# Kernel optimization log

Hardware: AMD Instinct MI355X
Metric: run time of the kernel (lower is better)

## Reference

```python
import jax, jax.numpy as jnp
import numpy as np
from itertools import combinations

N_QUBITS = 8
N_TRASH = 2
N_LAYERS = 4
BATCH = 32768
DIM = 2 ** N_QUBITS  # 256


def _cz_pairs():
    # same CZ pattern as layer() in the torch module; all pairs are distinct,
    # and CZ gates are diagonal and commute, so they fuse into one sign mask.
    pairs = list(combinations(range(N_TRASH), 2))
    for idx in range(N_TRASH):
        for i in range(N_TRASH):
            for j in range(N_TRASH + i, N_QUBITS, N_TRASH):
                pairs.append(((idx + i) % N_TRASH, j))
    return pairs


def _cz_layer_sign():
    bits = np.indices((2,) * N_QUBITS)  # [n_qubits, 2,...,2]; wire 0 = MSB (PennyLane order)
    sign = np.ones((2,) * N_QUBITS, np.float32)
    for a, b in _cz_pairs():
        sign = sign * (1.0 - 2.0 * (bits[a] * bits[b]).astype(np.float32))
    return jnp.asarray(sign)[None]  # broadcast over batch

_CZ_SIGN = _cz_layer_sign()


def _ry(state, theta, w):
    # RY(theta) on wire w, batched over leading axis. state: [B,2,...,2] complex64
    c = jnp.cos(theta / 2).astype(jnp.complex64)
    s = jnp.sin(theta / 2).astype(jnp.complex64)
    g = jnp.stack([jnp.stack([c, -s]), jnp.stack([s, c])])  # [2,2]
    out = jnp.tensordot(g, state, axes=((1,), (1 + w,)))
    return jnp.moveaxis(out, 0, 1 + w)


def _axis_vec(vals, w):
    shape = [1] * (N_QUBITS + 1)
    shape[1 + w] = 2
    return jnp.asarray(vals, dtype=jnp.complex64).reshape(shape)


def _apply_pauli(state, w, p):
    if p == 'X':
        return jnp.flip(state, axis=1 + w)
    if p == 'Y':
        return jnp.flip(state, axis=1 + w) * _axis_vec([-1j, 1j], w)
    return state * _axis_vec([1.0 + 0j, -1.0 + 0j], w)  # Z


def _forward(x, weights):
    # AmplitudeEmbedding(normalize=True)
    norm = jnp.sqrt(jnp.sum(x * x, axis=-1, keepdims=True))
    psi = (x / norm).astype(jnp.complex64).reshape((-1,) + (2,) * N_QUBITS)
    for l in range(N_LAYERS - 1):
        for q in range(N_QUBITS):
            psi = _ry(psi, weights[l * N_QUBITS + q], q)
        psi = psi * _CZ_SIGN  # all CZs of the layer fused into one diagonal
    base = (N_LAYERS - 1) * N_QUBITS
    for q in range(N_TRASH):  # last_layer: RY on trash qubits only
        psi = _ry(psi, weights[base + q], q)

    axes = tuple(range(1, N_QUBITS + 1))
    conj_psi = jnp.conj(psi)

    def ev(op_state):
        return jnp.sum(conj_psi * op_state, axis=axes).real.astype(jnp.float32)

    w0, w1 = 6, 7
    terms = [
        ev(_apply_pauli(psi, w0, 'X')),
        ev(_apply_pauli(psi, w0, 'Y')),
        ev(_apply_pauli(psi, w0, 'Z')),
        ev(_apply_pauli(psi, w1, 'X')),
        ev(_apply_pauli(psi, w1, 'Y')),
        ev(_apply_pauli(psi, w1, 'Z')),
        ev(_apply_pauli(_apply_pauli(psi, w0, 'X'), w1, 'X')),
        ev(_apply_pauli(_apply_pauli(psi, w0, 'Y'), w1, 'Y')),
        ev(_apply_pauli(_apply_pauli(psi, w0, 'Z'), w1, 'Z')),
    ]
    return jnp.stack(terms, axis=1)  # [B, 9]


def setup_inputs() -> dict:
    key = jax.random.key(0)
    kx, kw = jax.random.split(key)
    x = jax.random.normal(kx, (BATCH, DIM), dtype=jnp.float32)
    n_w = N_LAYERS * N_QUBITS - (N_QUBITS - N_TRASH)  # 26
    weights = jax.random.normal(kw, (n_w,), dtype=jnp.float32)
    return {'x': x, 'weights': weights}


def reference(x, weights):
    return _forward(x, weights)
```

## Files before the change

kernel.cpp:

```cpp
#include <hip/hip_runtime.h>
#include <math.h>

#define DIM 256
typedef float v2f  __attribute__((ext_vector_type(2)));
typedef _Float16 f16x8 __attribute__((ext_vector_type(8)));
typedef float f32x4 __attribute__((ext_vector_type(4)));

__device__ __forceinline__ v2f mk2(float a, float b) { v2f r; r.x = a; r.y = b; return r; }
__device__ __forceinline__ float rl(float v, int l) {
    return __uint_as_float(__builtin_amdgcn_readlane(__float_as_uint(v), l));
}

template<int B2>
__device__ __forceinline__ void ry_pk(v2f* v, float c, float s) {
#pragma unroll
    for (int p = 0; p < 16; ++p)
        if (!(p & (1 << B2))) {
            const int q = p | (1 << B2);
            v2f lo = v[p], hi = v[q];
            v[p] = c * lo - s * hi;
            v[q] = s * lo + c * hi;
        }
}
__device__ __forceinline__ void ry_intra(v2f* v, float c, float s) {
#pragma unroll
    for (int p = 0; p < 16; ++p) {
        float lo = v[p].x, hi = v[p].y;
        v[p].x = fmaf(-s, hi, c * lo);
        v[p].y = fmaf(s, lo, c * hi);
    }
}

__global__ __launch_bounds__(256) void qae_buildU(const float* __restrict__ w,
                                                  _Float16* __restrict__ uf) {
    __shared__ float4 lds4[2048];
    const int lane = threadIdx.x & 63;
    const int wid  = threadIdx.x >> 6;
    const int wave = blockIdx.x * 4 + wid;
    const int l3   = lane & 7;
    const int e    = lane >> 3;
    const int col  = wave * 8 + e;
    float4* W = lds4 + wid * 512 + e * 64;

    float h = 0.f;
    if (lane < 20) h = 0.5f * w[lane < 18 ? lane : lane + 4];
    const float cv = __cosf(h), sv = __sinf(h);
#define RYP(B2, slot) ry_pk<B2>(v, rl(cv, slot), rl(sv, slot))
#define RYI(slot)     ry_intra(v, rl(cv, slot), rl(sv, slot))

    const int a0 = (l3 >> 2) & 1, a1 = (l3 >> 1) & 1, a2 = l3 & 1;
    const int aa = a0 & a1, dd = a0 ^ a1;
    const float fE = (aa ^ (dd & a2)) ? -1.f : 1.f;
    const float fO = ((aa ^ (dd & a2)) ^ dd) ? -1.f : 1.f;
    const float pB = (__popc(l3) & 1) ? -1.f : 1.f;
    const v2f mA0 = mk2(fE, fO), mA1 = mk2(fO, fE);
    const v2f mBp = mk2(pB, -pB);

    v2f v[16];
#pragma unroll
    for (int p = 0; p < 16; ++p) v[p] = mk2(0.f, 0.f);
    if (((col >> 2) & 7) == l3) {
        const int p = 2 * (col >> 5) + ((col >> 1) & 1);
        if (col & 1) v[p].y = 1.f; else v[p].x = 1.f;
    }

    RYP(3, 0); RYP(2, 1); RYP(1, 2);
#pragma unroll
    for (int g = 0; g < 8; ++g)
        W[g * 8 + (l3 ^ g)] = make_float4(v[2*g].x, v[2*g].y, v[2*g+1].x, v[2*g+1].y);
#pragma unroll
    for (int k = 0; k < 8; ++k) {
        float4 f = W[l3 * 8 + (k ^ l3)];
        v[2*k] = mk2(f.x, f.y); v[2*k+1] = mk2(f.z, f.w);
    }
    RYP(3, 3); RYP(2, 4); RYP(1, 5); RYP(0, 6); RYI(7);
#pragma unroll
    for (int p = 0; p < 16; ++p) v[p] *= (__popc(p) & 1) ? mA1 : mA0;
    RYP(3, 11); RYP(2, 12); RYP(1, 13); RYP(0, 14); RYI(15);
#pragma unroll
    for (int k = 0; k < 8; ++k)
        W[l3 * 8 + (k ^ l3)] = make_float4(v[2*k].x, v[2*k].y, v[2*k+1].x, v[2*k+1].y);
#pragma unroll
    for (int g = 0; g < 8; ++g) {
        float4 f = W[g * 8 + (l3 ^ g)];
        v[2*g] = mk2(f.x, f.y); v[2*g+1] = mk2(f.z, f.w);
    }
    RYP(3, 8); RYP(2, 9); RYP(1, 10);
#pragma unroll
    for (int p = 0; p < 16; ++p) {
        const int b0 = (p >> 3) & 1, b1 = (p >> 2) & 1;
        if (b0 & b1)      v[p] = -v[p];
        else if (b0 ^ b1) v[p] *= (__popc(p & 3) & 1) ? -mBp : mBp;
    }
    RYP(3, 16); RYP(2, 17); RYP(0, 18); RYI(19);
#pragma unroll
    for (int p = 0; p < 16; ++p) {
        const int b0 = (p >> 3) & 1, b1 = (p >> 2) & 1;
        if (b0 & b1)      v[p] = -v[p];
        else if (b0 ^ b1) v[p] *= (__popc(p & 3) & 1) ? -mBp : mBp;
    }
#undef RYP
#undef RYI

    const int ks = col >> 5, j = col & 7, lfhi = ((col >> 3) & 3) << 4;
#pragma unroll
    for (int p = 0; p < 16; ++p) {
        const int mbase = ((p >> 1) << 5) | (l3 << 2) | ((p & 1) << 1);
        {   const int m = mbase, mt = m >> 4, lf = (m & 15) | lfhi;
            uf[(size_t)(((mt * 8 + ks) * 64 + lf) * 8 + j)] = (_Float16)v[p].x; }
        {   const int m = mbase | 1, mt = m >> 4, lf = (m & 15) | lfhi;
            uf[(size_t)(((mt * 8 + ks) * 64 + lf) * 8 + j)] = (_Float16)v[p].y; }
    }
}

__global__ __launch_bounds__(256) void qae_gemm(const float* __restrict__ x,
                                                const _Float16* __restrict__ uf,
                                                float* __restrict__ out, int batch) {
    __shared__ __align__(16) _Float16 Ut[16384];
    const int lane  = threadIdx.x & 63;
    const int wid   = threadIdx.x >> 6;
    const int strip = blockIdx.x * 4 + wid;
    const int bl = lane & 15, bq = lane >> 4;
    const int b  = strip * 16 + bl;
    const bool act = (b < batch);

    const float* xp = x + (size_t)b * DIM + bq * 8;
    f16x8 bf[8];
    float nrm = 0.f;
#pragma unroll
    for (int ks = 0; ks < 8; ++ks) {
        float4 f0 = make_float4(0.f, 0.f, 0.f, 0.f), f1 = f0;
        if (act) { f0 = *(const float4*)(xp + 32 * ks);
                   f1 = *(const float4*)(xp + 32 * ks + 4); }
        nrm += f0.x*f0.x + f0.y*f0.y + f0.z*f0.z + f0.w*f0.w
             + f1.x*f1.x + f1.y*f1.y + f1.z*f1.z + f1.w*f1.w;
        bf[ks][0] = (_Float16)f0.x; bf[ks][1] = (_Float16)f0.y;
        bf[ks][2] = (_Float16)f0.z; bf[ks][3] = (_Float16)f0.w;
        bf[ks][4] = (_Float16)f1.x; bf[ks][5] = (_Float16)f1.y;
        bf[ks][6] = (_Float16)f1.z; bf[ks][7] = (_Float16)f1.w;
    }

    float pX6 = 0, pX7 = 0, pXX = 0, pYY = 0, pZ6 = 0, pZ7 = 0, pZZ = 0;

#pragma unroll
    for (int ph = 0; ph < 4; ++ph) {
        __syncthreads();
        const float4* src = (const float4*)uf + (size_t)ph * 2048 + threadIdx.x;
        float4* dst = (float4*)Ut;
#pragma unroll
        for (int i = 0; i < 8; ++i)
            dst[i * 256 + threadIdx.x] = src[i * 256];
        __syncthreads();
#pragma unroll
        for (int mtl = 0; mtl < 4; ++mtl) {
            f32x4 acc = {0.f, 0.f, 0.f, 0.f};
#pragma unroll
            for (int ks = 0; ks < 8; ++ks) {
                f16x8 af = *(const f16x8*)(Ut + ((mtl * 8 + ks) * 64 + lane) * 8);
                acc = __builtin_amdgcn_mfma_f32_16x16x32_f16(af, bf[ks], acc, 0, 0, 0);
            }
            const float q0 = acc[0], q1 = acc[1], q2 = acc[2], q3 = acc[3];
            pX6 += q0 * q2 + q1 * q3;
            pX7 += q0 * q1 + q2 * q3;
            pXX += q0 * q3 + q1 * q2;
            pYY += q1 * q2 - q0 * q3;
            const float s0 = q0*q0, s1 = q1*q1, s2 = q2*q2, s3 = q3*q3;
            pZ6 += (s0 + s1) - (s2 + s3);
            pZ7 += (s0 - s1) + (s2 - s3);
            pZZ += (s0 - s1) - (s2 - s3);
        }
    }

#pragma unroll
    for (int m = 16; m <= 32; m <<= 1) {
        nrm += __shfl_xor(nrm, m);
        pX6 += __shfl_xor(pX6, m); pX7 += __shfl_xor(pX7, m);
        pXX += __shfl_xor(pXX, m); pYY += __shfl_xor(pYY, m);
        pZ6 += __shfl_xor(pZ6, m); pZ7 += __shfl_xor(pZ7, m);
        pZZ += __shfl_xor(pZZ, m);
    }

    if (act && bq == 0) {
        const float inv = 1.f / nrm;
        float* o = out + (size_t)b * 9;
        o[0] = 2.f * pX6 * inv;  o[1] = 0.f;  o[2] = pZ6 * inv;
        o[3] = 2.f * pX7 * inv;  o[4] = 0.f;  o[5] = pZ7 * inv;
        o[6] = 2.f * pXX * inv;  o[7] = 2.f * pYY * inv;  o[8] = pZZ * inv;
    }
}

extern "C" void kernel_launch(void* const* d_in, const int* in_sizes, int n_in,
                              void* d_out, int out_size, void* d_ws, size_t ws_size,
                              hipStream_t stream) {
    const float* x = (const float*)d_in[0];
    const float* w = (const float*)d_in[1];
    float* out = (float*)d_out;
    _Float16* uf = (_Float16*)d_ws;
    const int batch = in_sizes[0] / DIM;

    qae_buildU<<<8, 256, 0, stream>>>(w, uf);

    const int strips = (batch + 15) / 16;
    qae_gemm<<<(strips + 3) / 4, 256, 0, stream>>>(x, uf, out, batch);
}
```

Before: 92.63 us.

## Coalesce x loads through LDS staging and vectorize U-matrix fragment stores

The GEMM kernel now loads each 16-row strip of x with fully coalesced row-wise float4 reads, converts to fp16 into a per-wave LDS buffer, then reads the MFMA B fragments from LDS. Before, each lane read strided 32-byte pieces. The norm is now computed from the fp16-rounded values, a small accuracy change. buildU transposes its results through LDS so it can write 16-byte vector stores instead of scattered 2-byte stores. The change also sets launch_bounds occupancy to 2 and adds 32KB of LDS per block, which may limit occupancy.

```diff
diff --git a/kernel.cpp b/kernel.cpp
--- a/kernel.cpp
+++ b/kernel.cpp
@@ -4,6 +4,7 @@
 #define DIM 256
 typedef float v2f  __attribute__((ext_vector_type(2)));
 typedef _Float16 f16x8 __attribute__((ext_vector_type(8)));
+typedef _Float16 f16x4 __attribute__((ext_vector_type(4)));
 typedef float f32x4 __attribute__((ext_vector_type(4)));
 
 __device__ __forceinline__ v2f mk2(float a, float b) { v2f r; r.x = a; r.y = b; return r; }
@@ -102,42 +103,51 @@
 #undef RYP
 #undef RYI
 
-    const int ks = col >> 5, j = col & 7, lfhi = ((col >> 3) & 3) << 4;
-#pragma unroll
-    for (int p = 0; p < 16; ++p) {
-        const int mbase = ((p >> 1) << 5) | (l3 << 2) | ((p & 1) << 1);
-        {   const int m = mbase, mt = m >> 4, lf = (m & 15) | lfhi;
-            uf[(size_t)(((mt * 8 + ks) * 64 + lf) * 8 + j)] = (_Float16)v[p].x; }
-        {   const int m = mbase | 1, mt = m >> 4, lf = (m & 15) | lfhi;
-            uf[(size_t)(((mt * 8 + ks) * 64 + lf) * 8 + j)] = (_Float16)v[p].y; }
-    }
-}
-
-__global__ __launch_bounds__(256) void qae_gemm(const float* __restrict__ x,
-                                                const _Float16* __restrict__ uf,
-                                                float* __restrict__ out, int batch) {
+    _Float16* T = (_Float16*)(lds4 + wid * 512);
+#pragma unroll
+    for (int p = 0; p < 16; ++p) {
+        const int m0 = ((p >> 1) << 5) | (l3 << 2) | ((p & 1) << 1);
+        T[m0 * 8 + e]       = (_Float16)v[p].x;
+        T[(m0 + 1) * 8 + e] = (_Float16)v[p].y;
+    }
+    const int ksv = wave >> 2, lfh = (wave & 3) << 4;
+#pragma unroll
+    for (int i = 0; i < 4; ++i) {
+        const int m = lane * 4 + i;
+        const int mt = m >> 4, lf = (m & 15) | lfh;
+        f16x8 t = *(const f16x8*)(T + m * 8);
+        *(f16x8*)(uf + (size_t)(((mt * 8 + ksv) * 64 + lf) * 8)) = t;
+    }
+}
+
+__global__ __launch_bounds__(256, 2) void qae_gemm(const float* __restrict__ x,
+                                                   const _Float16* __restrict__ uf,
+                                                   float* __restrict__ out, int batch) {
+    __shared__ __align__(16) _Float16 Xs[4][4096];
     __shared__ __align__(16) _Float16 Ut[16384];
     const int lane  = threadIdx.x & 63;
     const int wid   = threadIdx.x >> 6;
     const int strip = blockIdx.x * 4 + wid;
     const int bl = lane & 15, bq = lane >> 4;
     const int b  = strip * 16 + bl;
-    const bool act = (b < batch);
-
-    const float* xp = x + (size_t)b * DIM + bq * 8;
+
+    _Float16* Xw = Xs[wid];
+#pragma unroll
+    for (int r = 0; r < 16; ++r) {
+        int gr = strip * 16 + r; if (gr >= batch) gr = batch - 1;
+        const float4 f = *(const float4*)(x + (size_t)gr * DIM + lane * 4);
+        f16x4 hh;
+        hh[0] = (_Float16)f.x; hh[1] = (_Float16)f.y;
+        hh[2] = (_Float16)f.z; hh[3] = (_Float16)f.w;
+        *(f16x4*)(Xw + r * 256 + lane * 4) = hh;
+    }
     f16x8 bf[8];
     float nrm = 0.f;
 #pragma unroll
     for (int ks = 0; ks < 8; ++ks) {
-        float4 f0 = make_float4(0.f, 0.f, 0.f, 0.f), f1 = f0;
-        if (act) { f0 = *(const float4*)(xp + 32 * ks);
-                   f1 = *(const float4*)(xp + 32 * ks + 4); }
-        nrm += f0.x*f0.x + f0.y*f0.y + f0.z*f0.z + f0.w*f0.w
-             + f1.x*f1.x + f1.y*f1.y + f1.z*f1.z + f1.w*f1.w;
-        bf[ks][0] = (_Float16)f0.x; bf[ks][1] = (_Float16)f0.y;
-        bf[ks][2] = (_Float16)f0.z; bf[ks][3] = (_Float16)f0.w;
-        bf[ks][4] = (_Float16)f1.x; bf[ks][5] = (_Float16)f1.y;
-        bf[ks][6] = (_Float16)f1.z; bf[ks][7] = (_Float16)f1.w;
+        bf[ks] = *(const f16x8*)(Xw + bl * 256 + ks * 32 + bq * 8);
+#pragma unroll
+        for (int j = 0; j < 8; ++j) { float t = (float)bf[ks][j]; nrm = fmaf(t, t, nrm); }
     }
 
     float pX6 = 0, pX7 = 0, pXX = 0, pYY = 0, pZ6 = 0, pZ7 = 0, pZZ = 0;
@@ -180,7 +190,7 @@
         pZZ += __shfl_xor(pZZ, m);
     }
 
-    if (act && bq == 0) {
+    if (b < batch && bq == 0) {
         const float inv = 1.f / nrm;
         float* o = out + (size_t)b * 9;
         o[0] = 2.f * pX6 * inv;  o[1] = 0.f;  o[2] = pZ6 * inv;
```

Measured after the change: 85.60 us. 1.08x faster.
